# Optimization experiments

Measured on AMD Instinct MI355X. Metric: run time of the kernel, lower is better.

Reference implementation:

```python
import jax, jax.numpy as jnp
import numpy as np
from jax import lax

INPUT_DIMS = [300, 74, 35]
HIDDEN_DIMS = [256, 64, 64]
OUT_CELL = 64
OUT_DIM = 1
B, T = 512, 128


def setup_inputs() -> dict:
    key = jax.random.key(0)
    ks = iter(jax.random.split(key, 32))
    d = {}
    for m, D in enumerate(INPUT_DIMS):
        d[f"x{m}"] = jax.random.normal(next(ks), (B, T, D), dtype=jnp.float32)
    s = 0.02
    for m, (D, H) in enumerate(zip(INPUT_DIMS, HIDDEN_DIMS)):
        d[f"w_ih{m}"] = jax.random.normal(next(ks), (4 * H, D), dtype=jnp.float32) * s
        d[f"w_hh{m}"] = jax.random.normal(next(ks), (4 * H, H), dtype=jnp.float32) * s
        d[f"b_ih{m}"] = jnp.zeros((4 * H,), dtype=jnp.float32)
        d[f"b_hh{m}"] = jnp.zeros((4 * H,), dtype=jnp.float32)
    sum_h = sum(HIDDEN_DIMS)
    d["w1"] = jax.random.normal(next(ks), (OUT_CELL, sum_h), dtype=jnp.float32) * s
    d["b1"] = jnp.zeros((OUT_CELL,), dtype=jnp.float32)
    d["w2"] = jax.random.normal(next(ks), (OUT_DIM, OUT_CELL), dtype=jnp.float32) * s
    d["b2"] = jnp.zeros((OUT_DIM,), dtype=jnp.float32)
    return d


def _lstm_last_h(x, w_ih, w_hh, b_ih, b_hh):
    # x: [B, T, D] -> last hidden state [B, H], torch.nn.LSTMCell gate order i,f,g,o
    Bsz = x.shape[0]
    H = w_hh.shape[1]
    xg = jnp.einsum("btd,gd->tbg", x, w_ih) + b_ih + b_hh  # precompute input projections [T,B,4H]

    def step(carry, xg_t):
        h, c = carry
        gates = xg_t + h @ w_hh.T
        i, f, g, o = jnp.split(gates, 4, axis=-1)
        c = jax.nn.sigmoid(f) * c + jax.nn.sigmoid(i) * jnp.tanh(g)
        h = jax.nn.sigmoid(o) * jnp.tanh(c)
        return (h, c), None

    h0 = jnp.zeros((Bsz, H), dtype=x.dtype)
    (h, _), _ = lax.scan(step, (h0, h0), xg)
    return h


def reference(x0, x1, x2,
              w_ih0, w_hh0, b_ih0, b_hh0,
              w_ih1, w_hh1, b_ih1, b_hh1,
              w_ih2, w_hh2, b_ih2, b_hh2,
              w1, b1, w2, b2):
    h0 = _lstm_last_h(x0, w_ih0, w_hh0, b_ih0, b_hh0)
    h1 = _lstm_last_h(x1, w_ih1, w_hh1, b_ih1, b_hh1)
    h2 = _lstm_last_h(x2, w_ih2, w_hh2, b_ih2, b_hh2)
    last_h = jnp.concatenate([h0, h1, h2], axis=1)  # [B, sum_h]
    hid = jax.nn.relu(last_h @ w1.T + b1)  # dropout = identity in eval
    return hid @ w2.T + b2  # [B, OUT_DIM]
```

## Files before the change

kernel.cpp:

```cpp
#include <hip/hip_runtime.h>

typedef _Float16 h8 __attribute__((ext_vector_type(8)));
typedef _Float16 h4 __attribute__((ext_vector_type(4)));
typedef float f4 __attribute__((ext_vector_type(4)));
typedef unsigned int u32x4 __attribute__((ext_vector_type(4)));
typedef unsigned long long u64;

__device__ __forceinline__ float sigm(float x) { return 1.f / (1.f + __expf(-x)); }
__device__ __forceinline__ float tanhf_(float x) { return 1.f - 2.f / (1.f + __expf(2.f * x)); }

__global__ __launch_bounds__(256) void pack_all(
    const float* __restrict__ wih0, const float* __restrict__ whh0,
    const float* __restrict__ wih1, const float* __restrict__ whh1,
    const float* __restrict__ wih2, const float* __restrict__ whh2,
    const float* __restrict__ bih0, const float* __restrict__ bhh0,
    const float* __restrict__ bih1, const float* __restrict__ bhh1,
    const float* __restrict__ bih2, const float* __restrict__ bhh2,
    _Float16* __restrict__ wihp0, _Float16* __restrict__ whhp0,
    _Float16* __restrict__ wihp1, _Float16* __restrict__ whhp1,
    _Float16* __restrict__ wihp2, _Float16* __restrict__ whhp2,
    float* __restrict__ biasc)
{
    if (blockIdx.x >= 324) {
        int bi = (blockIdx.x - 324) * 256 + threadIdx.x;
        if (bi < 1024)      biasc[bi] = bih0[bi] + bhh0[bi];
        else if (bi < 1280) biasc[bi] = bih1[bi - 1024] + bhh1[bi - 1024];
        else if (bi < 1536) biasc[bi] = bih2[bi - 1280] + bhh2[bi - 1280];
        return;
    }
    int s = blockIdx.x * 256 + threadIdx.x;
    const float* src; _Float16* dst; int KC, D;
    if (s < 40960)      {            dst = wihp0; src = wih0; KC = 10; D = 300; }
    else if (s < 73728) { s -= 40960; dst = whhp0; src = whh0; KC = 8;  D = 256; }
    else if (s < 76800) { s -= 73728; dst = wihp1; src = wih1; KC = 3;  D = 74;  }
    else if (s < 78848) { s -= 76800; dst = whhp1; src = whh1; KC = 2;  D = 64;  }
    else if (s < 80896) { s -= 78848; dst = wihp2; src = wih2; KC = 2;  D = 35;  }
    else                { s -= 80896; dst = whhp2; src = whh2; KC = 2;  D = 64;  }
    int lane = s & 63;
    int kc = (s >> 6) % KC;
    int gt = (s >> 6) / KC;
    int g = gt * 16 + (lane & 15);
    int kb = kc * 32 + ((lane >> 4) << 3);
    h8 v;
#pragma unroll
    for (int i = 0; i < 8; i++) {
        int k = kb + i;
        v[i] = (_Float16)((k < D) ? src[(size_t)g * D + k] : 0.f);
    }
    *(h8*)&dst[(size_t)s * 8] = v;
}

template <int M>
__device__ __forceinline__ void xg_block(int tc, int bq, int t0,
    const float* __restrict__ x, const _Float16* __restrict__ wihp,
    const float* __restrict__ bias, _Float16* __restrict__ xgp, _Float16* axf)
{
    constexpr int D   = (M == 0) ? 300 : ((M == 1) ? 74 : 35);
    constexpr int KCX = (M == 0) ? 10 : ((M == 1) ? 3 : 2);
    const int t = t0 + tc;
    const int tid = threadIdx.x, w = tid >> 6, l = tid & 63, ccol = l & 15;
    const int r0 = bq * 64;

    for (int sI = tid; sI < 4 * KCX * 64; sI += 512) {
        int rt = sI / (KCX * 64);
        int kc = (sI >> 6) % KCX;
        int ll = sI & 63;
        int row = r0 + rt * 16 + (ll & 15);
        int kb = kc * 32 + ((ll >> 4) << 3);
        const float* bp = x + ((size_t)row * 128 + t) * D + kb;
        h8 v;
#pragma unroll
        for (int i = 0; i < 8; i++) v[i] = (_Float16)((kb + i < D) ? bp[i] : 0.f);
        *(h8*)&axf[sI * 8] = v;
    }
    __syncthreads();

    if (M == 0) {
        f4 acc[4][8];
#pragma unroll
        for (int g = 0; g < 8; g++) {
            int gt = (g >> 1) * 16 + 2 * w + (g & 1);
            float b = bias[gt * 16 + ccol];
#pragma unroll
            for (int rt = 0; rt < 4; rt++) acc[rt][g] = (f4){b, b, b, b};
        }
#pragma unroll
        for (int kc = 0; kc < KCX; kc++) {
            h8 a[4];
#pragma unroll
            for (int rt = 0; rt < 4; rt++) a[rt] = *(const h8*)&axf[((rt * KCX + kc) * 64 + l) * 8];
#pragma unroll
            for (int g = 0; g < 8; g++) {
                int gt = (g >> 1) * 16 + 2 * w + (g & 1);
                h8 b = *(const h8*)&wihp[((size_t)(gt * KCX + kc) * 64 + l) * 8];
#pragma unroll
                for (int rt = 0; rt < 4; rt++)
                    acc[rt][g] = __builtin_amdgcn_mfma_f32_16x16x32_f16(a[rt], b, acc[rt][g], 0, 0, 0);
            }
        }
#pragma unroll
        for (int rtw = 0; rtw < 4; rtw++) {
            int gr = bq * 2 + (rtw >> 1), rt = rtw & 1;
#pragma unroll
            for (int gi = 0; gi < 8; gi++) {
                int ga = gi >> 1;
                int e = 2 * w + (gi & 1);
                int s2 = e >> 2;
                int w2 = (e & 3) * 2 + rt;
                f4 a = acc[rtw][gi];
                h4 v;
#pragma unroll
                for (int q = 0; q < 4; q++) v[q] = (_Float16)a[q];
                size_t off = (size_t)tc * 524288 +
                             ((((size_t)gr * 4 + s2) * 8 + w2) * 64 + l) * 16 + ga * 4;
                *(h4*)&xgp[off] = v;
            }
        }
    } else {
        const int rh = w >> 2, ht = w & 3;
        f4 acc[2][4];
#pragma unroll
        for (int ga = 0; ga < 4; ga++) {
            int gt = ga * 4 + ht;
            float b = bias[gt * 16 + ccol];
            acc[0][ga] = (f4){b, b, b, b};
            acc[1][ga] = (f4){b, b, b, b};
        }
#pragma unroll
        for (int kc = 0; kc < KCX; kc++) {
            h8 a[2];
#pragma unroll
            for (int rr = 0; rr < 2; rr++)
                a[rr] = *(const h8*)&axf[(((rh * 2 + rr) * KCX + kc) * 64 + l) * 8];
#pragma unroll
            for (int ga = 0; ga < 4; ga++) {
                int gt = ga * 4 + ht;
                h8 b = *(const h8*)&wihp[((size_t)(gt * KCX + kc) * 64 + l) * 8];
#pragma unroll
                for (int rr = 0; rr < 2; rr++)
                    acc[rr][ga] = __builtin_amdgcn_mfma_f32_16x16x32_f16(a[rr], b, acc[rr][ga], 0, 0, 0);
            }
        }
#pragma unroll
        for (int rr = 0; rr < 2; rr++)
#pragma unroll
        for (int gp = 0; gp < 2; gp++) {
            f4 lo = acc[rr][2 * gp], hi = acc[rr][2 * gp + 1];
            h8 v;
#pragma unroll
            for (int q = 0; q < 4; q++) { v[q] = (_Float16)lo[q]; v[4 + q] = (_Float16)hi[q]; }
            int fp = rr * 2 + gp;
            size_t off = ((((size_t)tc * 8 + bq) * 8 + w) * 4 + fp) * 64 + l;
            *(h8*)&xgp[off * 8] = v;
        }
    }
}

__global__ __launch_bounds__(512, 2) void xg_kernel(
    const float* __restrict__ x0, const float* __restrict__ x1, const float* __restrict__ x2,
    const _Float16* __restrict__ wihp0, const _Float16* __restrict__ wihp1,
    const _Float16* __restrict__ wihp2, const float* __restrict__ biasc,
    _Float16* __restrict__ xgp0, _Float16* __restrict__ xgp1, _Float16* __restrict__ xgp2,
    int t0, int TC)
{
    __shared__ __align__(16) _Float16 axf[4 * 10 * 64 * 8];
    int b = blockIdx.x;
    int per = TC * 8;
    if (b < per)            xg_block<0>(b >> 3, b & 7, t0, x0, wihp0, biasc,        xgp0, axf);
    else if (b < 2 * per) { b -= per;     xg_block<1>(b >> 3, b & 7, t0, x1, wihp1, biasc + 1024, xgp1, axf); }
    else                  { b -= 2 * per; xg_block<2>(b >> 3, b & 7, t0, x2, wihp2, biasc + 1280, xgp2, axf); }
}

__global__ __launch_bounds__(512, 1) void rec_kernel(
    const _Float16* __restrict__ whhp0, const _Float16* __restrict__ whhp1,
    const _Float16* __restrict__ whhp2,
    const _Float16* __restrict__ xgp0, const _Float16* __restrict__ xgp1,
    const _Float16* __restrict__ xgp2,
    float* __restrict__ h_all, float* __restrict__ csave, _Float16* __restrict__ hsave,
    u64* __restrict__ hx, int* __restrict__ ctr,
    int t0, int TC)
{
    __shared__ __align__(16) char smem[151552];
    const int bid = blockIdx.x;
    const int tid = threadIdx.x, w = tid >> 6, l = tid & 63;
    const int ccol = l & 15, crow = (l >> 4) * 4;

    if (bid < 64) {
        const int g = bid & 15, s = bid >> 4;
        const int r0 = g * 32;
        _Float16* whhs   = (_Float16*)smem;
        _Float16* apack  = (_Float16*)(smem + 131072);
        _Float16* hstage = (_Float16*)(smem + 147456);
        const int hgroup = w >> 1, rt = w & 1;

        for (int v = tid; v < 8192; v += 512) {
            int gtl = v >> 9, off = v & 511;
            int gt = (gtl >> 2) * 16 + s * 4 + (gtl & 3);
            ((u32x4*)whhs)[v] = ((const u32x4*)whhp0)[(size_t)gt * 512 + off];
        }
        float c[4];
        float* cs = csave + ((size_t)bid * 512 + tid) * 4;
        if (t0 == 0) {
#pragma unroll
            for (int i = 0; i < 4; i++) c[i] = 0.f;
            u32x4 z = (u32x4){0u, 0u, 0u, 0u};
            for (int v = tid; v < 1024; v += 512) ((u32x4*)apack)[v] = z;
        } else {
#pragma unroll
            for (int i = 0; i < 4; i++) c[i] = cs[i];
            for (int v = tid; v < 2048; v += 512)
                ((u64*)apack)[v] = __hip_atomic_load(&hx[((size_t)(t0 - 1) * 16 + g) * 2048 + v],
                                                     __ATOMIC_RELAXED, __HIP_MEMORY_SCOPE_AGENT);
        }
        __syncthreads();

        const _Float16* xgb = xgp0 + ((((size_t)g * 4 + s) * 8 + w) * 64 + l) * 16;
        h8 xcur0 = *(const h8*)&xgb[0];
        h8 xcur1 = *(const h8*)&xgb[8];

        f4 acc[4];
        for (int tc = 0; tc < TC; tc++) {
            const int t = t0 + tc;
#pragma unroll
            for (int q = 0; q < 4; q++) {
                acc[0][q] = (float)xcur0[q];
                acc[1][q] = (float)xcur0[4 + q];
                acc[2][q] = (float)xcur1[q];
                acc[3][q] = (float)xcur1[4 + q];
            }
            h8 xn0 = xcur0, xn1 = xcur1;
            if (tc + 1 < TC) {
                xn0 = *(const h8*)&xgb[(size_t)(tc + 1) * 524288];
                xn1 = *(const h8*)&xgb[(size_t)(tc + 1) * 524288 + 8];
            }
#pragma unroll
            for (int kc = 0; kc < 8; kc++) {
                h8 a = *(const h8*)&apack[((kc * 2 + rt) * 64 + l) * 8];
#pragma unroll
                for (int ga = 0; ga < 4; ga++) {
                    h8 b = *(const h8*)&whhs[(((ga * 4 + hgroup) * 8 + kc) * 64 + l) * 8];
                    acc[ga] = __builtin_amdgcn_mfma_f32_16x16x32_f16(a, b, acc[ga], 0, 0, 0);
                }
            }
#pragma unroll
            for (int q = 0; q < 4; q++) {
                float gi = acc[0][q], gf = acc[1][q], gg = acc[2][q], go = acc[3][q];
                float cn = sigm(gf) * c[q] + sigm(gi) * tanhf_(gg);
                c[q] = cn;
                float hv = sigm(go) * tanhf_(cn);
                int row = rt * 16 + crow + q;
                int hcol = hgroup * 16 + ccol;
                if (t == 127) {
                    h_all[(size_t)(r0 + row) * 384 + s * 64 + hcol] = hv;
                } else {
                    int lane2 = (((hcol & 31) >> 3) << 4) | (row & 15);
                    hstage[(((hcol >> 5) * 2 + rt) * 64 + lane2) * 8 + (l & 7)] = (_Float16)hv;
                }
            }
            xcur0 = xn0; xcur1 = xn1;
            __syncthreads();
            if (t < 127) {
                u64 hval = ((u64*)hstage)[tid];
                __hip_atomic_store(&hx[(((size_t)t * 16 + g) * 4 + s) * 512 + tid], hval,
                                   __ATOMIC_RELAXED, __HIP_MEMORY_SCOPE_AGENT);
                __syncthreads();
                if (tid == 0) {
                    int old = __hip_atomic_fetch_add(&ctr[t * 16 + g], 1,
                                                     __ATOMIC_RELAXED, __HIP_MEMORY_SCOPE_AGENT);
                    if (old < 3)
                        while (__hip_atomic_load(&ctr[t * 16 + g],
                                                 __ATOMIC_RELAXED, __HIP_MEMORY_SCOPE_AGENT) < 4) {}
                }
                __syncthreads();
                for (int v = tid; v < 2048; v += 512)
                    ((u64*)apack)[v] = __hip_atomic_load(&hx[((size_t)t * 16 + g) * 2048 + v],
                                                         __ATOMIC_RELAXED, __HIP_MEMORY_SCOPE_AGENT);
                __syncthreads();
            }
        }
        if (t0 + TC < 128) {
#pragma unroll
            for (int i = 0; i < 4; i++) cs[i] = c[i];
        }
    } else {
        const int m = (bid < 72) ? 1 : 2;
        const int lb = (bid - 64) & 7;
        const int r0 = lb * 64;
        const int colb = (m == 1) ? 256 : 320;
        const _Float16* whhp = (m == 1) ? whhp1 : whhp2;
        const _Float16* xgp  = (m == 1) ? xgp1 : xgp2;
        _Float16* whhs = (_Float16*)smem;
        _Float16* apkA = (_Float16*)(smem + 32768);
        _Float16* apkB = (_Float16*)(smem + 40960);
        const int rh = w >> 2, ht = w & 3;
        float c[8];
        h8 xbuf[4];
        float* cs = csave + 131072 + (((size_t)(bid - 64)) * 512 + tid) * 8;
        for (int v = tid; v < 2048; v += 512) ((u32x4*)whhs)[v] = ((const u32x4*)whhp)[v];
        if (t0 == 0) {
#pragma unroll
            for (int i = 0; i < 8; i++) c[i] = 0.f;
            u32x4 z = (u32x4){0u, 0u, 0u, 0u};
            for (int v = tid; v < 512; v += 512) ((u32x4*)apkA)[v] = z;
        } else {
#pragma unroll
            for (int i = 0; i < 8; i++) c[i] = cs[i];
            const u32x4* hsrc = (const u32x4*)(hsave + (size_t)(bid - 64) * 4096);
            for (int v = tid; v < 512; v += 512) ((u32x4*)apkA)[v] = hsrc[v];
        }
        __syncthreads();

        const size_t xbase = ((size_t)lb * 8 + w) * 4 * 512 + (size_t)l * 8;
#pragma unroll
        for (int fp = 0; fp < 4; fp++)
            xbuf[fp] = *(const h8*)&xgp[xbase + (size_t)fp * 512];

        f4 acc[2][4];
        for (int tc = 0; tc < TC; tc++) {
            _Float16* cur = (tc & 1) ? apkB : apkA;
            _Float16* nxt = (tc & 1) ? apkA : apkB;
#pragma unroll
            for (int rr = 0; rr < 2; rr++)
#pragma unroll
            for (int gp = 0; gp < 2; gp++) {
                int fp = rr * 2 + gp;
#pragma unroll
                for (int q = 0; q < 4; q++) {
                    acc[rr][2 * gp][q]     = (float)xbuf[fp][q];
                    acc[rr][2 * gp + 1][q] = (float)xbuf[fp][4 + q];
                }
            }
            if (tc + 1 < TC) {
                size_t nb = xbase + (size_t)(tc + 1) * 8 * 8 * 4 * 512;
#pragma unroll
                for (int fp = 0; fp < 4; fp++)
                    xbuf[fp] = *(const h8*)&xgp[nb + (size_t)fp * 512];
            }
#pragma unroll
            for (int kc = 0; kc < 2; kc++) {
                h8 a0 = *(const h8*)&cur[(((rh * 2 + 0) * 2 + kc) * 64 + l) * 8];
                h8 a1 = *(const h8*)&cur[(((rh * 2 + 1) * 2 + kc) * 64 + l) * 8];
#pragma unroll
                for (int ga = 0; ga < 4; ga++) {
                    int gt = ga * 4 + ht;
                    h8 b = *(const h8*)&whhs[((gt * 2 + kc) * 64 + l) * 8];
                    acc[0][ga] = __builtin_amdgcn_mfma_f32_16x16x32_f16(a0, b, acc[0][ga], 0, 0, 0);
                    acc[1][ga] = __builtin_amdgcn_mfma_f32_16x16x32_f16(a1, b, acc[1][ga], 0, 0, 0);
                }
            }
            const int t = t0 + tc;
#pragma unroll
            for (int rr = 0; rr < 2; rr++)
#pragma unroll
            for (int q = 0; q < 4; q++) {
                int idx = rr * 4 + q;
                float gi = acc[rr][0][q];
                float gf = acc[rr][1][q];
                float gg = acc[rr][2][q];
                float go = acc[rr][3][q];
                float cn = sigm(gf) * c[idx] + sigm(gi) * tanhf_(gg);
                c[idx] = cn;
                float hv = sigm(go) * tanhf_(cn);
                int row = (rh * 2 + rr) * 16 + crow + q;
                int hcol = ht * 16 + ccol;
                if (t == 127) h_all[(size_t)(r0 + row) * 384 + colb + hcol] = hv;
                int kch = ht >> 1;
                int sub = (ht & 1) * 2 + (ccol >> 3);
                nxt[(((row >> 4) * 2 + kch) * 64 + sub * 16 + (row & 15)) * 8 + (ccol & 7)] = (_Float16)hv;
            }
            __syncthreads();
        }
        if (t0 + TC < 128) {
#pragma unroll
            for (int i = 0; i < 8; i++) cs[i] = c[i];
            u32x4* hdst = (u32x4*)(hsave + (size_t)(bid - 64) * 4096);
            const u32x4* src = (const u32x4*)((TC & 1) ? apkB : apkA);
            for (int v = tid; v < 512; v += 512) hdst[v] = src[v];
        }
    }
}

__global__ __launch_bounds__(512) void mlp_kernel(const float* __restrict__ h_all,
                                                  const float* __restrict__ w1,
                                                  const float* __restrict__ b1,
                                                  const float* __restrict__ w2,
                                                  const float* __restrict__ b2,
                                                  float* __restrict__ out)
{
    __shared__ float w1s[64 * 385];
    __shared__ float hs[8 * 384];
    int tid = threadIdx.x;
    for (int idx = tid; idx < 64 * 384; idx += 512) {
        int j = idx / 384, k = idx - j * 384;
        w1s[j * 385 + k] = w1[idx];
    }
    int r0 = blockIdx.x * 8;
    for (int idx = tid; idx < 8 * 384; idx += 512) hs[idx] = h_all[(size_t)r0 * 384 + idx];
    __syncthreads();

    int w = tid >> 6, j = tid & 63;
    float accv = b1[j];
    const float* hrow = &hs[w * 384];
    for (int k = 0; k < 384; k++) accv = fmaf(hrow[k], w1s[j * 385 + k], accv);
    float hid = fmaxf(accv, 0.f);
    float v = hid * w2[j];
#pragma unroll
    for (int off = 32; off >= 1; off >>= 1) v += __shfl_xor(v, off, 64);
    if (j == 0) out[r0 + w] = v + b2[0];
}

extern "C" void kernel_launch(void* const* d_in, const int* in_sizes, int n_in,
                              void* d_out, int out_size, void* d_ws, size_t ws_size,
                              hipStream_t stream)
{
    const float* x0   = (const float*)d_in[0];
    const float* x1   = (const float*)d_in[1];
    const float* x2   = (const float*)d_in[2];
    const float* wih0 = (const float*)d_in[3];
    const float* whh0 = (const float*)d_in[4];
    const float* bih0 = (const float*)d_in[5];
    const float* bhh0 = (const float*)d_in[6];
    const float* wih1 = (const float*)d_in[7];
    const float* whh1 = (const float*)d_in[8];
    const float* bih1 = (const float*)d_in[9];
    const float* bhh1 = (const float*)d_in[10];
    const float* wih2 = (const float*)d_in[11];
    const float* whh2 = (const float*)d_in[12];
    const float* bih2 = (const float*)d_in[13];
    const float* bhh2 = (const float*)d_in[14];
    const float* w1   = (const float*)d_in[15];
    const float* b1   = (const float*)d_in[16];
    const float* w2   = (const float*)d_in[17];
    const float* b2   = (const float*)d_in[18];

    char* ws = (char*)d_ws;
    size_t off = 0;
    auto alloc = [&](size_t bytes) { size_t o = off; off = (off + bytes + 255) & ~255ULL; return o; };
    size_t o_wihp0 = alloc(655360);
    size_t o_whhp0 = alloc(524288);
    size_t o_wihp1 = alloc(49152);
    size_t o_whhp1 = alloc(32768);
    size_t o_wihp2 = alloc(32768);
    size_t o_whhp2 = alloc(32768);
    size_t o_bias  = alloc(6144);
    size_t o_hall  = alloc(786432);
    size_t o_csave = alloc(786432);
    size_t o_hsave = alloc(131072);
    size_t o_hx    = alloc(33554432);
    size_t o_ctr   = alloc(8192);
    size_t fixed = off;

    int TC = 128;
    while (TC > 1 && fixed + (size_t)TC * 1572864ULL + 1024 > ws_size) TC >>= 1;
    size_t o_xgp0 = alloc((size_t)TC * 1048576ULL);
    size_t o_xgp1 = alloc((size_t)TC * 262144ULL);
    size_t o_xgp2 = alloc((size_t)TC * 262144ULL);

    _Float16* wihp0 = (_Float16*)(ws + o_wihp0);
    _Float16* whhp0 = (_Float16*)(ws + o_whhp0);
    _Float16* wihp1 = (_Float16*)(ws + o_wihp1);
    _Float16* whhp1 = (_Float16*)(ws + o_whhp1);
    _Float16* wihp2 = (_Float16*)(ws + o_wihp2);
    _Float16* whhp2 = (_Float16*)(ws + o_whhp2);
    float*    biasc = (float*)(ws + o_bias);
    float*    hall  = (float*)(ws + o_hall);
    float*    csave = (float*)(ws + o_csave);
    _Float16* hsave = (_Float16*)(ws + o_hsave);
    u64*      hx    = (u64*)(ws + o_hx);
    int*      ctr   = (int*)(ws + o_ctr);
    _Float16* xgp0  = (_Float16*)(ws + o_xgp0);
    _Float16* xgp1  = (_Float16*)(ws + o_xgp1);
    _Float16* xgp2  = (_Float16*)(ws + o_xgp2);

    hipMemsetAsync(ws + o_ctr, 0, 8192, stream);

    pack_all<<<330, 256, 0, stream>>>(wih0, whh0, wih1, whh1, wih2, whh2,
                                      bih0, bhh0, bih1, bhh1, bih2, bhh2,
                                      wihp0, whhp0, wihp1, whhp1, wihp2, whhp2, biasc);

    for (int t0 = 0; t0 < 128; t0 += TC) {
        xg_kernel<<<24 * TC, 512, 0, stream>>>(x0, x1, x2, wihp0, wihp1, wihp2, biasc,
                                               xgp0, xgp1, xgp2, t0, TC);
        rec_kernel<<<80, 512, 0, stream>>>(whhp0, whhp1, whhp2, xgp0, xgp1, xgp2,
                                           hall, csave, hsave, hx, ctr, t0, TC);
    }

    mlp_kernel<<<64, 512, 0, stream>>>(hall, w1, b1, w2, b2, (float*)d_out);
}
```

Baseline: 645.1 us.

## Replace counter barrier with per-block flags and all-thread polling in LSTM0 exchange

The four blocks sharing an LSTM0 row group now each set their own flag instead of doing an atomic fetch-add on one counter. Every thread polls the three peer flags, which removes one __syncthreads and the single-thread spin. Each block writes its own h slice straight into shared memory and loads only the three peer slices from global memory, cutting the per-step reload. The risk is more polling traffic from all 512 threads, and the flag writes and hx stores use relaxed ordering with no fence between them.

Measured after the change: 571.2 us. -11.5%, faster.

```diff
diff --git a/kernel.cpp b/kernel.cpp
--- a/kernel.cpp
+++ b/kernel.cpp
@@ -5,6 +5,7 @@
 typedef float f4 __attribute__((ext_vector_type(4)));
 typedef unsigned int u32x4 __attribute__((ext_vector_type(4)));
 typedef unsigned long long u64;
+typedef unsigned int u32;
 
 __device__ __forceinline__ float sigm(float x) { return 1.f / (1.f + __expf(-x)); }
 __device__ __forceinline__ float tanhf_(float x) { return 1.f - 2.f / (1.f + __expf(2.f * x)); }
@@ -177,7 +178,7 @@
     const _Float16* __restrict__ xgp0, const _Float16* __restrict__ xgp1,
     const _Float16* __restrict__ xgp2,
     float* __restrict__ h_all, float* __restrict__ csave, _Float16* __restrict__ hsave,
-    u64* __restrict__ hx, int* __restrict__ ctr,
+    u64* __restrict__ hx, u32* __restrict__ flags,
     int t0, int TC)
 {
     __shared__ __align__(16) char smem[151552];
@@ -191,7 +192,9 @@
         _Float16* whhs   = (_Float16*)smem;
         _Float16* apack  = (_Float16*)(smem + 131072);
         _Float16* hstage = (_Float16*)(smem + 147456);
+        u64* apack_u64   = (u64*)apack;
         const int hgroup = w >> 1, rt = w & 1;
+        const int s1 = (s + 1) & 3, s2 = (s + 2) & 3, s3 = (s + 3) & 3;
 
         for (int v = tid; v < 8192; v += 512) {
             int gtl = v >> 9, off = v & 511;
@@ -209,8 +212,8 @@
 #pragma unroll
             for (int i = 0; i < 4; i++) c[i] = cs[i];
             for (int v = tid; v < 2048; v += 512)
-                ((u64*)apack)[v] = __hip_atomic_load(&hx[((size_t)(t0 - 1) * 16 + g) * 2048 + v],
-                                                     __ATOMIC_RELAXED, __HIP_MEMORY_SCOPE_AGENT);
+                apack_u64[v] = __hip_atomic_load(&hx[((size_t)(t0 - 1) * 16 + g) * 2048 + v],
+                                                 __ATOMIC_RELAXED, __HIP_MEMORY_SCOPE_AGENT);
         }
         __syncthreads();
 
@@ -263,18 +266,25 @@
                 u64 hval = ((u64*)hstage)[tid];
                 __hip_atomic_store(&hx[(((size_t)t * 16 + g) * 4 + s) * 512 + tid], hval,
                                    __ATOMIC_RELAXED, __HIP_MEMORY_SCOPE_AGENT);
+                apack_u64[s * 512 + tid] = hval;
                 __syncthreads();
-                if (tid == 0) {
-                    int old = __hip_atomic_fetch_add(&ctr[t * 16 + g], 1,
-                                                     __ATOMIC_RELAXED, __HIP_MEMORY_SCOPE_AGENT);
-                    if (old < 3)
-                        while (__hip_atomic_load(&ctr[t * 16 + g],
-                                                 __ATOMIC_RELAXED, __HIP_MEMORY_SCOPE_AGENT) < 4) {}
+                if (tid == 0)
+                    __hip_atomic_store(&flags[((size_t)t * 16 + g) * 32 + s], 1u,
+                                       __ATOMIC_RELAXED, __HIP_MEMORY_SCOPE_AGENT);
+                const u32* fl = &flags[((size_t)t * 16 + g) * 32];
+                while (true) {
+                    u32 fa = __hip_atomic_load(&fl[s1], __ATOMIC_RELAXED, __HIP_MEMORY_SCOPE_AGENT);
+                    u32 fb = __hip_atomic_load(&fl[s2], __ATOMIC_RELAXED, __HIP_MEMORY_SCOPE_AGENT);
+                    u32 fc = __hip_atomic_load(&fl[s3], __ATOMIC_RELAXED, __HIP_MEMORY_SCOPE_AGENT);
+                    if (fa + fb + fc == 3u) break;
                 }
-                __syncthreads();
-                for (int v = tid; v < 2048; v += 512)
-                    ((u64*)apack)[v] = __hip_atomic_load(&hx[((size_t)t * 16 + g) * 2048 + v],
-                                                         __ATOMIC_RELAXED, __HIP_MEMORY_SCOPE_AGENT);
+                const u64* hxs = &hx[(((size_t)t * 16 + g) * 4) * 512];
+                u64 v1 = __hip_atomic_load(&hxs[s1 * 512 + tid], __ATOMIC_RELAXED, __HIP_MEMORY_SCOPE_AGENT);
+                u64 v2 = __hip_atomic_load(&hxs[s2 * 512 + tid], __ATOMIC_RELAXED, __HIP_MEMORY_SCOPE_AGENT);
+                u64 v3 = __hip_atomic_load(&hxs[s3 * 512 + tid], __ATOMIC_RELAXED, __HIP_MEMORY_SCOPE_AGENT);
+                apack_u64[s1 * 512 + tid] = v1;
+                apack_u64[s2 * 512 + tid] = v2;
+                apack_u64[s3 * 512 + tid] = v3;
                 __syncthreads();
             }
         }
@@ -447,7 +457,7 @@
     size_t o_csave = alloc(786432);
     size_t o_hsave = alloc(131072);
     size_t o_hx    = alloc(33554432);
-    size_t o_ctr   = alloc(8192);
+    size_t o_flags = alloc(262144);
     size_t fixed = off;
 
     int TC = 128;
@@ -467,12 +477,12 @@
     float*    csave = (float*)(ws + o_csave);
     _Float16* hsave = (_Float16*)(ws + o_hsave);
     u64*      hx    = (u64*)(ws + o_hx);
-    int*      ctr   = (int*)(ws + o_ctr);
+    u32*      flags = (u32*)(ws + o_flags);
     _Float16* xgp0  = (_Float16*)(ws + o_xgp0);
     _Float16* xgp1  = (_Float16*)(ws + o_xgp1);
     _Float16* xgp2  = (_Float16*)(ws + o_xgp2);
 
-    hipMemsetAsync(ws + o_ctr, 0, 8192, stream);
+    hipMemsetAsync(ws + o_flags, 0, 262144, stream);
 
     pack_all<<<330, 256, 0, stream>>>(wih0, whh0, wih1, whh1, wih2, whh2,
                                       bih0, bhh0, bih1, bhh1, bih2, bhh2,
@@ -482,7 +492,7 @@
         xg_kernel<<<24 * TC, 512, 0, stream>>>(x0, x1, x2, wihp0, wihp1, wihp2, biasc,
                                                xgp0, xgp1, xgp2, t0, TC);
         rec_kernel<<<80, 512, 0, stream>>>(whhp0, whhp1, whhp2, xgp0, xgp1, xgp2,
-                                           hall, csave, hsave, hx, ctr, t0, TC);
+                                           hall, csave, hsave, hx, flags, t0, TC);
     }
 
     mlp_kernel<<<64, 512, 0, stream>>>(hall, w1, b1, w2, b2, (float*)d_out);
```
